# Performance work log

Hardware: AMD Instinct MI355X
Metric: run time of the kernel (lower is better)

## Reference

```python
import jax, jax.numpy as jnp
import numpy as np

B, S, D = 4, 2048, 1024


def setup_inputs() -> dict:
    key = jax.random.key(0)
    k1, k2, k3 = jax.random.split(key, 3)
    x = jax.random.normal(k1, (B, S, D), dtype=jnp.float32)
    # torch nn.Linear weights are [out_features, in_features]
    wq_w = jax.random.normal(k2, (D, D), dtype=jnp.float32) * (1.0 / np.sqrt(D))
    wv_w = jax.random.normal(k3, (D, D), dtype=jnp.float32) * (1.0 / np.sqrt(D))
    return {"x": x, "wq_w": wq_w, "wv_w": wv_w}


def reference(x, wq_w, wv_w):
    b, s, d = x.shape
    q = x @ wq_w.T                      # [B,S,D]
    kv = x @ wv_w.T                     # [B,S,D]  (original uses wv for BOTH k and v; wk unused)
    # original: k.view(B, k_dim, -1) -- a raw memory RESHAPE, not a transpose
    k_r = kv.reshape(b, d, s)           # [B,D,S]
    scores = jnp.einsum('bsd,bdt->bst', q, k_r) / np.sqrt(d)  # [B,S,S]
    sm = jax.nn.softmax(scores, axis=-1)
    sm = jnp.tril(sm)                   # post-softmax causal mask (rows NOT renormalized)
    return jnp.einsum('bst,btd->bsd', sm, kv)
```

## Files before the change

### kernel.cpp

```cpp
#include <hip/hip_runtime.h>


typedef __attribute__((ext_vector_type(8))) _Float16 f16x8;
typedef __attribute__((ext_vector_type(4))) _Float16 f16x4;
typedef __attribute__((ext_vector_type(4))) float f32x4;

__device__ __forceinline__ void glds16(const void* g, void* l) {
  __builtin_amdgcn_global_load_lds((const __attribute__((address_space(1))) void*)g,
                                   (__attribute__((address_space(3))) void*)l, 16, 0, 0);
}
#define BAR() __builtin_amdgcn_s_barrier()
#define LGKM0() do { asm volatile("s_waitcnt lgkmcnt(0)" ::: "memory"); \
                     __builtin_amdgcn_sched_barrier(0); } while (0)
#define VM2() asm volatile("s_waitcnt vmcnt(2)" ::: "memory")
#define VM0() asm volatile("s_waitcnt vmcnt(0)" ::: "memory")
#define PR1() __builtin_amdgcn_s_setprio(1)
#define PR0() __builtin_amdgcn_s_setprio(0)

__device__ __forceinline__ unsigned pkh2(float a, float b) {
  union { _Float16 h[2]; unsigned u; } c;
  c.h[0] = (_Float16)a; c.h[1] = (_Float16)b;
  return c.u;
}

__global__ __launch_bounds__(256) void cvt3(const float* __restrict__ x,
                                            const float* __restrict__ wq,
                                            const float* __restrict__ wv,
                                            _Float16* __restrict__ xh,
                                            _Float16* __restrict__ wqh,
                                            _Float16* __restrict__ wvh) {
  int i = blockIdx.x * 256 + threadIdx.x;
  const float* src;
  _Float16* dst;
  int off;
  if (i < 2097152) { src = x; dst = xh; off = i; }
  else if (i < 2359296) { src = wq; dst = wqh; off = i - 2097152; }
  else { src = wv; dst = wvh; off = i - 2359296; }
  float4 v = ((const float4*)src)[off];
  f16x4 o = {(_Float16)v.x, (_Float16)v.y, (_Float16)v.z, (_Float16)v.w};
  ((f16x4*)dst)[off] = o;
}

template <typename OUT_T, int EPI>
__global__ __launch_bounds__(512, 2) void gemm8p(const _Float16* __restrict__ A,
                                                 const _Float16* __restrict__ BT,
                                                 OUT_T* __restrict__ C,
                                                 _Float16* __restrict__ T1,
                                                 _Float16* __restrict__ T2,
                                                 int K, int ldc,
                                                 long sA, long sB, long sC, float scale,
                                                 int lgx, int lgy) {
  extern __shared__ char smem[];
  _Float16* lds = (_Float16*)smem;
  const int lin = blockIdx.x + gridDim.x * (blockIdx.y + gridDim.y * blockIdx.z);
  const int xcd = lin & 7, s = lin >> 3;
  const int G = (gridDim.y * gridDim.z) >> 3;
  const int mx = s & ((1 << lgx) - 1);
  const int pid = xcd * G + (s >> lgx);
  const int ny = pid & (gridDim.y - 1);
  const int bz = pid >> lgy;
  A += (size_t)bz * sA;
  BT += (size_t)bz * sB;
  C += (size_t)bz * sC;
  const int m0 = mx << 8, n0 = ny << 8;
  const int tid = threadIdx.x, lane = tid & 63, wave = tid >> 6;
  const int wm = wave >> 2, wn = wave & 3;
  const int lr = lane & 15, lk = lane >> 4, xr = lane & 7;
  const int nkt = K >> 6;
  const int A0 = 0, A1 = 8192, B0 = 16384, B1 = 24576, BUF = 32768;
  const int baseA = wm ? A1 : A0;
  const int baseB = B0 + ((wn >> 1) << 13);
  const int bRow = (wn & 1) << 6;
  const int srow = lane >> 3;
  const int scolB = ((lane & 7) << 4) ^ (srow << 4);

  f32x4 acc[8][4] = {};
  f16x8 fa[4][2], fb[4][2];

#define STAGE(bufsel, halfsel, G_, hrow0, kt) do {                                   \
    const _Float16* _g = (G_) + (size_t)((hrow0) + wave * 16 + srow) * K + ((kt) << 6); \
    glds16((const char*)_g + scolB, (char*)&lds[(bufsel) * BUF + (halfsel) + wave * 1024]); \
    glds16((const char*)(_g + (size_t)8 * K) + scolB,                                \
           (char*)&lds[(bufsel) * BUF + (halfsel) + wave * 1024 + 512]);             \
  } while (0)
#define RDA(buf, mf, ks) (*(const f16x8*)&lds[(buf) * BUF + baseA + ((mf) * 16 + lr) * 64 + \
                                              ((((ks) * 4 + lk) ^ xr) << 3)])
#define RDB(buf, nf, ks) (*(const f16x8*)&lds[(buf) * BUF + baseB + (bRow + (nf) * 16 + lr) * 64 + \
                                              ((((ks) * 4 + lk) ^ xr) << 3)])
#define RDFA4(b, mbase) do { _Pragma("unroll")                                        \
    for (int i = 0; i < 4; ++i) { fa[i][0] = RDA(b, (mbase) + i, 0);                  \
                                  fa[i][1] = RDA(b, (mbase) + i, 1); } } while (0)
#define RDFB2(b, jbase) do { _Pragma("unroll")                                        \
    for (int j = 0; j < 2; ++j) { fb[(jbase) + j][0] = RDB(b, (jbase) + j, 0);        \
                                  fb[(jbase) + j][1] = RDB(b, (jbase) + j, 1); } } while (0)
#define MMQ(ib, jb) do { _Pragma("unroll")                                            \
    for (int i = 0; i < 4; ++i) { _Pragma("unroll")                                   \
      for (int j = 0; j < 2; ++j) {                                                   \
        acc[(ib) + i][(jb) + j] = __builtin_amdgcn_mfma_f32_16x16x32_f16(             \
            fa[i][0], fb[(jb) + j][0], acc[(ib) + i][(jb) + j], 0, 0, 0);             \
        acc[(ib) + i][(jb) + j] = __builtin_amdgcn_mfma_f32_16x16x32_f16(             \
            fa[i][1], fb[(jb) + j][1], acc[(ib) + i][(jb) + j], 0, 0, 0);             \
      } } } while (0)

  STAGE(0, A0, A, m0, 0);
  STAGE(0, A1, A, m0 + 128, 0);
  STAGE(0, B0, BT, n0, 0);
  STAGE(0, B1, BT, n0 + 128, 0);
  STAGE(1, A0, A, m0, 1);
  VM2();
  BAR();

  for (int it = 0; it < (nkt >> 1); ++it) {
    const int t = it << 1;
    const int t2 = (t + 2 < nkt) ? t + 2 : 0;
    const int t3 = (t + 3 < nkt) ? t + 3 : 0;
    RDFA4(0, 0); RDFB2(0, 0);
    STAGE(1, A1, A, m0 + 128, t + 1);
    STAGE(1, B0, BT, n0, t + 1);
    BAR(); LGKM0(); PR1(); MMQ(0, 0); PR0(); BAR();
    RDFB2(0, 2);
    STAGE(1, B1, BT, n0 + 128, t + 1);
    BAR(); LGKM0(); PR1(); MMQ(0, 2); PR0(); BAR();
    RDFA4(0, 4);
    BAR(); LGKM0(); PR1(); MMQ(4, 2); PR0(); BAR();
    STAGE(0, A0, A, m0, t2);
    VM2();
    BAR(); PR1(); MMQ(4, 0); PR0(); BAR();
    RDFA4(1, 0); RDFB2(1, 0);
    STAGE(0, A1, A, m0 + 128, t2);
    STAGE(0, B0, BT, n0, t2);
    BAR(); LGKM0(); PR1(); MMQ(0, 0); PR0(); BAR();
    RDFB2(1, 2);
    STAGE(0, B1, BT, n0 + 128, t2);
    BAR(); LGKM0(); PR1(); MMQ(0, 2); PR0(); BAR();
    RDFA4(1, 4);
    BAR(); LGKM0(); PR1(); MMQ(4, 2); PR0(); BAR();
    STAGE(1, A0, A, m0, t3);
    VM2();
    BAR(); PR1(); MMQ(4, 0); PR0(); BAR();
  }

  if (EPI == 1 && bz == 1) {
    const int b = m0 >> 11;
    _Float16* kvvT = T1 + ((size_t)b << 21);
    _Float16* kvT  = T2 + ((size_t)b << 21);
    const int tb = (m0 & 2047) + wm * 128;
    const int db = n0 + wn * 64;
    char* wlds = smem + wave * 16384;
#pragma unroll
    for (int mf = 0; mf < 8; ++mf)
#pragma unroll
      for (int nf = 0; nf < 4; ++nf) {
        const int tl = mf * 16 + lk * 4;
        const int dl = nf * 16 + lr;
        const f32x4 a = acc[mf][nf];
        uint2 w = {pkh2(a[0], a[1]), pkh2(a[2], a[3])};
        *(uint2*)(wlds + dl * 256 + ((tl * 2) ^ ((dl & 7) << 4))) = w;
      }
#pragma unroll
    for (int it2 = 0; it2 < 32; ++it2) {
      const int dl = it2 * 2 + (lane >> 5);
      const int d = db + dl;
      const int tseg = (lane & 31) * 4;
      uint2 v = *(const uint2*)(wlds + dl * 256 + ((tseg * 2) ^ ((dl & 7) << 4)));
      *(uint2*)(kvT + (size_t)d * 2048 + tb + tseg) = v;
      unsigned ev = (v.x & 0xFFFFu) | (v.y << 16);
      unsigned od = (v.x >> 16) | (v.y & 0xFFFF0000u);
      const int k0 = (tb + tseg) >> 1;
      *(unsigned*)(kvvT + (size_t)d * 1024 + k0) = ev;
      *(unsigned*)(kvvT + (size_t)(1024 + d) * 1024 + k0) = od;
    }
  } else if (EPI == 2) {
    float* Pst = (float*)T1 + (size_t)bz * 2048 * 32;
    const int gidx = ny * 4 + wn;
    const bool wr = (n0 <= m0);
#pragma unroll
    for (int mf = 0; mf < 8; ++mf) {
      float e[4][4];
#pragma unroll
      for (int nf = 0; nf < 4; ++nf)
#pragma unroll
        for (int r = 0; r < 4; ++r)
          e[nf][r] = __expf(acc[mf][nf][r] * scale - 8.0f);
      const int row = m0 + wm * 128 + mf * 16 + lk * 4;
#pragma unroll
      for (int r = 0; r < 4; ++r) {
        float sm = (e[0][r] + e[1][r]) + (e[2][r] + e[3][r]);
#pragma unroll
        for (int off = 1; off < 16; off <<= 1) sm += __shfl_xor(sm, off);
        if (lr == 0) Pst[(size_t)(row + r) * 32 + gidx] = sm;
      }
      if (wr) {
#pragma unroll
        for (int nf = 0; nf < 4; ++nf) {
          const int col = n0 + wn * 64 + nf * 16 + lr;
#pragma unroll
          for (int r = 0; r < 4; ++r)
            C[(size_t)(row + r) * ldc + col] =
                (OUT_T)((col <= row + r) ? e[nf][r] : 0.f);
        }
      }
    }
  } else {
#pragma unroll
    for (int mf = 0; mf < 8; ++mf)
#pragma unroll
      for (int nf = 0; nf < 4; ++nf) {
        const int row = m0 + wm * 128 + mf * 16 + lk * 4;
        const int col = n0 + wn * 64 + nf * 16 + lr;
#pragma unroll
        for (int r = 0; r < 4; ++r)
          C[(size_t)(row + r) * ldc + col] = (OUT_T)(acc[mf][nf][r] * scale);
      }
  }
#undef STAGE
#undef RDA
#undef RDB
#undef RDFA4
#undef RDFB2
#undef MMQ
}

__global__ __launch_bounds__(256) void stats_combine(const float* __restrict__ Pst,
                                                     float* __restrict__ St) {
  const int row = blockIdx.x * 256 + threadIdx.x;
  const float4* p = (const float4*)(Pst + (size_t)row * 32);
  float l = 0.f;
#pragma unroll
  for (int g = 0; g < 8; ++g) {
    float4 v = p[g];
    l += (v.x + v.y) + (v.z + v.w);
  }
  St[row] = 1.f / l;
}

__global__ __launch_bounds__(256) void gemm_pv_bal(const _Float16* __restrict__ P,
                                                   const _Float16* __restrict__ KVT,
                                                   const float* __restrict__ St,
                                                   float* __restrict__ Out,
                                                   long sA, long sB, long sC) {
  __shared__ _Float16 As[2][64 * 64];
  __shared__ _Float16 Bs[2][128 * 64];
  const int total = gridDim.x * gridDim.y * gridDim.z;
  int lin = blockIdx.x + gridDim.x * (blockIdx.y + gridDim.y * blockIdx.z);
  const int xcd = lin & 7, slot = lin >> 3;
  const int perx = total >> 7;
  const int grp = xcd * perx + (slot >> 4);
  const int p = slot & 15;
  const int ny = grp & 7, bz = grp >> 3;
  P += (size_t)bz * sA;
  KVT += (size_t)bz * sB;
  Out += (size_t)bz * sC;
  St += (size_t)bz * 2048;
  const int n0 = ny * 128;
  const int lane = threadIdx.x & 63, wave = threadIdx.x >> 6;
  const int fr = lane & 15, lk = lane >> 4;
  const int srow = lane >> 3;
  const int scol = (((lane & 7) ^ srow) << 4);

#define PSTAGE(buf, m0s, t) do {                                                     \
    const int _k0 = (t) << 6;                                                        \
    _Pragma("unroll")                                                                \
    for (int c = 0; c < 2; ++c) {                                                    \
      const int ch = wave * 2 + c;                                                   \
      glds16((const char*)(P + (size_t)((m0s) + ch * 8 + srow) * 2048 + _k0) + scol, \
             &As[buf][ch * 512]);                                                    \
    }                                                                                \
    _Pragma("unroll")                                                                \
    for (int c = 0; c < 4; ++c) {                                                    \
      const int ch = wave * 4 + c;                                                   \
      glds16((const char*)(KVT + (size_t)(n0 + ch * 8 + srow) * 2048 + _k0) + scol,  \
             &Bs[buf][ch * 512]);                                                    \
    }                                                                                \
  } while (0)

#pragma unroll
  for (int half = 0; half < 2; ++half) {
    const int strip = half ? (31 - p) : p;
    const int m0s = strip * 64;
    const int nt = strip + 1;
    f32x4 acc[4][2] = {};
    PSTAGE(0, m0s, 0);
    VM0();
    BAR();
    for (int t = 0; t < nt; ++t) {
      const int cur = t & 1;
      if (t + 1 < nt) PSTAGE(cur ^ 1, m0s, t + 1);
      f16x8 af[4][2], bf[2][2];
#pragma unroll
      for (int m = 0; m < 4; ++m) {
        const int r = m * 16 + fr;
#pragma unroll
        for (int ks = 0; ks < 2; ++ks)
          af[m][ks] = *(const f16x8*)&As[cur][r * 64 + (((ks * 4 + lk) ^ (r & 7)) << 3)];
      }
#pragma unroll
      for (int n = 0; n < 2; ++n) {
        const int rb = wave * 32 + n * 16 + fr;
#pragma unroll
        for (int ks = 0; ks < 2; ++ks)
          bf[n][ks] = *(const f16x8*)&Bs[cur][rb * 64 + (((ks * 4 + lk) ^ (rb & 7)) << 3)];
      }
      LGKM0();
      PR1();
#pragma unroll
      for (int ks = 0; ks < 2; ++ks)
#pragma unroll
        for (int m = 0; m < 4; ++m)
#pragma unroll
          for (int n = 0; n < 2; ++n)
            acc[m][n] = __builtin_amdgcn_mfma_f32_16x16x32_f16(af[m][ks], bf[n][ks],
                                                               acc[m][n], 0, 0, 0);
      PR0();
      VM0();
      BAR();
    }
#pragma unroll
    for (int m = 0; m < 4; ++m) {
      const int row = m0s + m * 16 + lk * 4;
      float cr[4];
#pragma unroll
      for (int r = 0; r < 4; ++r) cr[r] = St[row + r];
#pragma unroll
      for (int n = 0; n < 2; ++n) {
        const int col = n0 + wave * 32 + n * 16 + fr;
#pragma unroll
        for (int r = 0; r < 4; ++r)
          Out[(size_t)(row + r) * 1024 + col] = acc[m][n][r] * cr[r];
      }
    }
  }
#undef PSTAGE
}

extern "C" void kernel_launch(void* const* d_in, const int* in_sizes, int n_in,
                              void* d_out, int out_size, void* d_ws, size_t ws_size,
                              hipStream_t stream) {
  const float* x = (const float*)d_in[0];
  const float* wq = (const float*)d_in[1];
  const float* wv = (const float*)d_in[2];
  float* out = (float*)d_out;
  char* ws = (char*)d_ws;

  const size_t MB = 1024 * 1024;
  const int bc = (ws_size >= 88 * MB) ? 4 : 2;
  const size_t scBytes = (size_t)bc * 2048 * 2048 * 2;
  const long PB = 2048 * 1024;
  const long SB = (long)2048 * 2048;

  _Float16* Sc = (_Float16*)ws;
  _Float16* qh = (_Float16*)(ws + scBytes);
  _Float16* kvvT = (_Float16*)(ws + scBytes + 16 * MB);
  _Float16* kvT = (_Float16*)(ws + scBytes + 32 * MB);
  _Float16* wqh = (_Float16*)(ws + scBytes + 48 * MB);
  _Float16* wvh = (_Float16*)(ws + scBytes + 50 * MB);
  float* Pst = (float*)(ws + scBytes + 52 * MB);
  float* Stt = (float*)(ws + scBytes + 53 * MB + 512 * 1024);
  _Float16* xh = (_Float16*)ws;

  cvt3<<<10240, 256, 0, stream>>>(x, wq, wv, xh, wqh, wvh);

  gemm8p<_Float16, 1><<<dim3(32, 4, 2), 512, 131072, stream>>>(
      xh, wqh, qh, kvvT, kvT, 1024, 1024, 0, (long)(wvh - wqh), 0, 1.0f, 5, 2);

  for (int b0 = 0; b0 < 4; b0 += bc) {
    gemm8p<_Float16, 2><<<dim3(8, 8, bc), 512, 131072, stream>>>(
        qh + (size_t)b0 * PB, kvvT + (size_t)b0 * PB, Sc, (_Float16*)Pst, nullptr,
        1024, 2048, PB, PB, SB, 0.03125f, 3, 3);
    stats_combine<<<bc * 8, 256, 0, stream>>>(Pst, Stt);
    gemm_pv_bal<<<dim3(16, 8, bc), 256, 0, stream>>>(
        Sc, kvT + (size_t)b0 * PB, Stt, out + (size_t)b0 * PB, SB, PB, PB);
  }
}
```

Before: 128.7 us.

## Fuse softmax row-stat combine into PV GEMM and remap projection GEMM tiles

Removes the separate stats_combine kernel. Each PV block now sums the 32 partial softmax denominators for its 64-row strip itself, stores the reciprocals in LDS and reads them in the epilogue. This saves one kernel launch and a global round trip per batch chunk, at the cost of some redundant partial-sum loads across the column blocks. The projection GEMM (EPI==1) also gets a fixed XCD-aware mapping so that neighbouring m-tiles, which share rows of A, run on the same XCD for better L2 reuse.

After: 122.5 us. 4.8% less time.

```diff
diff --git a/kernel.cpp b/kernel.cpp
--- a/kernel.cpp
+++ b/kernel.cpp
@@ -14,6 +14,7 @@
                      __builtin_amdgcn_sched_barrier(0); } while (0)
 #define VM2() asm volatile("s_waitcnt vmcnt(2)" ::: "memory")
 #define VM0() asm volatile("s_waitcnt vmcnt(0)" ::: "memory")
+#define VMLG0() asm volatile("s_waitcnt vmcnt(0) lgkmcnt(0)" ::: "memory")
 #define PR1() __builtin_amdgcn_s_setprio(1)
 #define PR0() __builtin_amdgcn_s_setprio(0)
 
@@ -54,11 +55,19 @@
   _Float16* lds = (_Float16*)smem;
   const int lin = blockIdx.x + gridDim.x * (blockIdx.y + gridDim.y * blockIdx.z);
   const int xcd = lin & 7, s = lin >> 3;
-  const int G = (gridDim.y * gridDim.z) >> 3;
-  const int mx = s & ((1 << lgx) - 1);
-  const int pid = xcd * G + (s >> lgx);
-  const int ny = pid & (gridDim.y - 1);
-  const int bz = pid >> lgy;
+  int mx, ny, bz;
+  if (EPI == 1) {
+    mx = (xcd << 2) | (s >> 3);
+    const int nyz = s & 7;
+    ny = nyz & 3;
+    bz = nyz >> 2;
+  } else {
+    const int G = (gridDim.y * gridDim.z) >> 3;
+    mx = s & ((1 << lgx) - 1);
+    const int pid = xcd * G + (s >> lgx);
+    ny = pid & (gridDim.y - 1);
+    bz = pid >> lgy;
+  }
   A += (size_t)bz * sA;
   BT += (size_t)bz * sB;
   C += (size_t)bz * sC;
@@ -221,26 +230,14 @@
 #undef MMQ
 }
 
-__global__ __launch_bounds__(256) void stats_combine(const float* __restrict__ Pst,
-                                                     float* __restrict__ St) {
-  const int row = blockIdx.x * 256 + threadIdx.x;
-  const float4* p = (const float4*)(Pst + (size_t)row * 32);
-  float l = 0.f;
-#pragma unroll
-  for (int g = 0; g < 8; ++g) {
-    float4 v = p[g];
-    l += (v.x + v.y) + (v.z + v.w);
-  }
-  St[row] = 1.f / l;
-}
-
 __global__ __launch_bounds__(256) void gemm_pv_bal(const _Float16* __restrict__ P,
                                                    const _Float16* __restrict__ KVT,
-                                                   const float* __restrict__ St,
+                                                   const float* __restrict__ Pst,
                                                    float* __restrict__ Out,
                                                    long sA, long sB, long sC) {
   __shared__ _Float16 As[2][64 * 64];
   __shared__ _Float16 Bs[2][128 * 64];
+  __shared__ float StL[2][64];
   const int total = gridDim.x * gridDim.y * gridDim.z;
   int lin = blockIdx.x + gridDim.x * (blockIdx.y + gridDim.y * blockIdx.z);
   const int xcd = lin & 7, slot = lin >> 3;
@@ -251,9 +248,10 @@
   P += (size_t)bz * sA;
   KVT += (size_t)bz * sB;
   Out += (size_t)bz * sC;
-  St += (size_t)bz * 2048;
+  Pst += (size_t)bz * 2048 * 32;
   const int n0 = ny * 128;
-  const int lane = threadIdx.x & 63, wave = threadIdx.x >> 6;
+  const int tid = threadIdx.x;
+  const int lane = tid & 63, wave = tid >> 6;
   const int fr = lane & 15, lk = lane >> 4;
   const int srow = lane >> 3;
   const int scol = (((lane & 7) ^ srow) << 4);
@@ -279,9 +277,19 @@
     const int strip = half ? (31 - p) : p;
     const int m0s = strip * 64;
     const int nt = strip + 1;
+    if (tid < 64) {
+      const float4* pp = (const float4*)(Pst + (size_t)(m0s + tid) * 32);
+      float l = 0.f;
+#pragma unroll
+      for (int g = 0; g < 8; ++g) {
+        float4 v = pp[g];
+        l += (v.x + v.y) + (v.z + v.w);
+      }
+      StL[half][tid] = 1.f / l;
+    }
     f32x4 acc[4][2] = {};
     PSTAGE(0, m0s, 0);
-    VM0();
+    VMLG0();
     BAR();
     for (int t = 0; t < nt; ++t) {
       const int cur = t & 1;
@@ -317,10 +325,11 @@
     }
 #pragma unroll
     for (int m = 0; m < 4; ++m) {
-      const int row = m0s + m * 16 + lk * 4;
+      const int rl = m * 16 + lk * 4;
+      const int row = m0s + rl;
       float cr[4];
 #pragma unroll
-      for (int r = 0; r < 4; ++r) cr[r] = St[row + r];
+      for (int r = 0; r < 4; ++r) cr[r] = StL[half][rl + r];
 #pragma unroll
       for (int n = 0; n < 2; ++n) {
         const int col = n0 + wave * 32 + n * 16 + fr;
@@ -355,7 +364,6 @@
   _Float16* wqh = (_Float16*)(ws + scBytes + 48 * MB);
   _Float16* wvh = (_Float16*)(ws + scBytes + 50 * MB);
   float* Pst = (float*)(ws + scBytes + 52 * MB);
-  float* Stt = (float*)(ws + scBytes + 53 * MB + 512 * 1024);
   _Float16* xh = (_Float16*)ws;
 
   cvt3<<<10240, 256, 0, stream>>>(x, wq, wv, xh, wqh, wvh);
@@ -367,8 +375,7 @@
     gemm8p<_Float16, 2><<<dim3(8, 8, bc), 512, 131072, stream>>>(
         qh + (size_t)b0 * PB, kvvT + (size_t)b0 * PB, Sc, (_Float16*)Pst, nullptr,
         1024, 2048, PB, PB, SB, 0.03125f, 3, 3);
-    stats_combine<<<bc * 8, 256, 0, stream>>>(Pst, Stt);
     gemm_pv_bal<<<dim3(16, 8, bc), 256, 0, stream>>>(
-        Sc, kvT + (size_t)b0 * PB, Stt, out + (size_t)b0 * PB, SB, PB, PB);
-  }
-}
+        Sc, kvT + (size_t)b0 * PB, Pst, out + (size_t)b0 * PB, SB, PB, PB);
+  }
+}
```
